# Optimization experiments

Measured on AMD Instinct MI355X. Metric: run time of the kernel, lower is better.

The kernel has to match this reference:

```python
import jax, jax.numpy as jnp
import numpy as np
import math

B, T, D = 2, 1024, 256
N, H = 1024, 8
HD = N // H
K = 32
STEPS = 2
VOCAB = 32000
TWO_PI = 2.0 * math.pi


def _ln(x, g, b):
    mu = x.mean(-1, keepdims=True)
    var = ((x - mu) ** 2).mean(-1, keepdims=True)
    return (x - mu) / jnp.sqrt(var + 1e-5) * g + b


def _gelu(x):
    # torch nn.GELU default = exact erf form
    return jax.nn.gelu(x, approximate=False)


def _forward(tokens, emb, field_init, Wq, Wv, mW1, mb1, mW2, mb2, base_metric,
             decoder, hebbian, fW1, fb1, fW2, fb2, g1, b1, g2, b2, gf, bf, Wl, bl):
    x = emb[tokens] + field_init  # [B,T,D]
    # quantized RoPE (BDH): freqs quantized in pairs, phases mod 1
    freqs = 1.0 / (2.0 ** 16) ** (jnp.floor(jnp.arange(D) / 2) * 2.0 / D) / TWO_PI  # [D]
    phases = (jnp.arange(T, dtype=jnp.float32)[:, None] * freqs[None, :]) % 1.0 * TWO_PI  # [T,D]
    cos, sin = jnp.cos(phases)[None], jnp.sin(phases)[None]
    x_rot = jnp.stack([-x[..., 1::2], x[..., ::2]], axis=-1).reshape(x.shape)
    x = x * cos + x_rot * sin

    # window j of token t covers padded positions t..t+K-1 == original t-(K-1)..t (causal)
    win_idx = jnp.arange(T)[:, None] + jnp.arange(K)[None, :]  # [T,K]

    def interaction(y):
        qs = jax.nn.relu(jnp.einsum('btd,hde->bthe', y, Wq))  # [B,T,H,HD] sparse query
        vs = jax.nn.relu(jnp.einsum('btd,hde->bthe', y, Wv))  # [B,T,H,HD] sparse value
        # dynamic diagonal metric from field signature
        qf = qs.reshape(B, T, N)
        sig = qf.mean(1) + qf[:, ::8].mean(1) * 0.5  # T >= 8 branch
        mod = _gelu(sig @ mW1 + mb1) @ mW2 + mb2  # [B,H*HD]
        metric = jax.nn.softplus(base_metric[None] + 0.1 * mod.reshape(B, H, HD)) + 1e-6
        # causal k-window extraction (unfold equivalent)
        qp = jnp.pad(qs, ((0, 0), (K - 1, 0), (0, 0), (0, 0)))
        vp = jnp.pad(vs, ((0, 0), (K - 1, 0), (0, 0), (0, 0)))
        qw = qp[:, win_idx].transpose(0, 1, 3, 2, 4)  # [B,T,H,K,HD]
        vw = vp[:, win_idx].transpose(0, 1, 3, 2, 4)
        diff = qs[:, :, :, None, :] - qw
        dist = jnp.sqrt(jnp.sum(metric[:, None, :, None, :] * diff ** 2, -1) + 1e-8)  # [B,T,H,K]
        infl = jnp.exp(-dist)
        infl = infl / (infl.sum(-1, keepdims=True) + 1e-8)
        ctx = jnp.einsum('bthk,bthkd->bthd', infl, vw)
        # Hebbian memory contraction (eval mode: state is fixed buffer)
        qn = qs / jnp.maximum(jnp.linalg.norm(qs, axis=-1, keepdims=True), 1e-12)
        ctx = ctx + jnp.einsum('bthd,hde->bthe', qn, hebbian)
        # multiplicative gating + decode
        return (qs * ctx).reshape(B, T, N) @ decoder

    for _ in range(STEPS):  # fixed evolution steps (eval, dropout off)
        dx = interaction(_ln(x, g1, b1)) + (_gelu(_ln(x, g2, b2) @ fW1 + fb1) @ fW2 + fb2)
        x = x + dx
    return _ln(x, gf, bf) @ Wl + bl  # [B,T,VOCAB]


def setup_inputs() -> dict:
    key = jax.random.key(0)
    ks = jax.random.split(key, 12)
    s = 0.02
    return {
        'tokens': jax.random.randint(ks[0], (B, T), 0, VOCAB),
        'emb': jax.random.normal(ks[1], (VOCAB, D)) * s,
        'field_init': jax.random.normal(ks[2], (1, 1, D)) * s,
        'Wq': jax.random.normal(ks[3], (H, D, HD)) * s,
        'Wv': jax.random.normal(ks[4], (H, D, HD)) * s,
        'mW1': jax.random.normal(ks[5], (N, N // 2)) * s,
        'mb1': jnp.zeros((N // 2,)),
        'mW2': jax.random.normal(ks[6], (N // 2, H * HD)) * s,
        'mb2': jnp.zeros((H * HD,)),
        'base_metric': jnp.ones((H, HD)) * 0.1,
        'decoder': jax.random.normal(ks[7], (N, D)) * s,
        'hebbian': jax.random.normal(ks[8], (H, HD, HD)) * 0.01,
        'fW1': jax.random.normal(ks[9], (D, 4 * D)) * s,
        'fb1': jnp.zeros((4 * D,)),
        'fW2': jax.random.normal(ks[10], (4 * D, D)) * s,
        'fb2': jnp.zeros((D,)),
        'g1': jnp.ones((D,)), 'b1': jnp.zeros((D,)),
        'g2': jnp.ones((D,)), 'b2': jnp.zeros((D,)),
        'gf': jnp.ones((D,)), 'bf': jnp.zeros((D,)),
        'Wl': jax.random.normal(ks[11], (D, VOCAB)) * s,
        'bl': jnp.zeros((VOCAB,)),
    }


def reference(tokens, emb, field_init, Wq, Wv, mW1, mb1, mW2, mb2, base_metric,
              decoder, hebbian, fW1, fb1, fW2, fb2, g1, b1, g2, b2, gf, bf, Wl, bl):
    return _forward(tokens, emb, field_init, Wq, Wv, mW1, mb1, mW2, mb2, base_metric,
                    decoder, hebbian, fW1, fb1, fW2, fb2, g1, b1, g2, b2, gf, bf, Wl, bl)
```

## Files before the change

### kernel.cpp

```cpp
#include <hip/hip_runtime.h>
#include <hip/hip_bf16.h>
#include <math.h>

#define B_ 2
#define T_ 1024
#define D_ 256
#define N_ 1024
#define H_ 8
#define HD_ 128
#define K_ 32
#define VOCAB_ 32000
#define TC_ 16

typedef __attribute__((ext_vector_type(8))) short short8v;
typedef __attribute__((ext_vector_type(4))) float f32x4;

static __device__ __forceinline__ float geluf(float x) {
    return 0.5f * x * (1.0f + erff(x * 0.70710678118654752f));
}

static __device__ __forceinline__ ushort f2bf(float f) {
    unsigned u = __builtin_bit_cast(unsigned, f);
    u += 0x7fff + ((u >> 16) & 1);
    return (ushort)(u >> 16);
}

static __device__ __forceinline__ float bf2f(ushort u) {
    unsigned v = ((unsigned)u) << 16;
    return __builtin_bit_cast(float, v);
}

__global__ void embed_rope_ln_kernel(const int* __restrict__ tokens,
                                     const float* __restrict__ emb,
                                     const float* __restrict__ field_init,
                                     const float* __restrict__ g1, const float* __restrict__ b1,
                                     const float* __restrict__ g2, const float* __restrict__ b2,
                                     float* __restrict__ x,
                                     ushort* __restrict__ y1, ushort* __restrict__ y2) {
    int bt = blockIdx.x;
    int d = threadIdx.x;
    int t = bt & (T_ - 1);
    int tok = tokens[bt];
    float v = emb[(long)tok * D_ + d] + field_init[d];
    float partner = __shfl_xor(v, 1);
    float rot = (d & 1) ? partner : -partner;
    float freq = exp2f(-0.0625f * (float)(d & ~1)) * (1.0f / 6.283185307179586f);
    float ph = fmodf((float)t * freq, 1.0f) * 6.283185307179586f;
    v = v * cosf(ph) + rot * sinf(ph);
    long i = (long)bt * D_ + d;
    x[i] = v;
    __shared__ float red[4];
    int lane = d & 63, wid = d >> 6;
    float s = v;
    #pragma unroll
    for (int off = 32; off; off >>= 1) s += __shfl_xor(s, off);
    if (lane == 0) red[wid] = s;
    __syncthreads();
    float mu = (red[0] + red[1] + red[2] + red[3]) * (1.0f / D_);
    float dv = v - mu;
    float s2 = dv * dv;
    #pragma unroll
    for (int off = 32; off; off >>= 1) s2 += __shfl_xor(s2, off);
    __syncthreads();
    if (lane == 0) red[wid] = s2;
    __syncthreads();
    float var = (red[0] + red[1] + red[2] + red[3]) * (1.0f / D_);
    float rstd = rsqrtf(var + 1e-5f);
    float nv = dv * rstd;
    y1[i] = f2bf(nv * g1[d] + b1[d]);
    y2[i] = f2bf(nv * g2[d] + b2[d]);
}

__global__ void ln_kernel(float* __restrict__ x,
                          const float* __restrict__ addA, const float* __restrict__ addB,
                          const float* __restrict__ g1, const float* __restrict__ b1,
                          const float* __restrict__ g2, const float* __restrict__ b2,
                          ushort* __restrict__ y1, ushort* __restrict__ y2) {
    int row = blockIdx.x;
    int d = threadIdx.x;
    long i = (long)row * D_ + d;
    float v = x[i] + addA[i] + addB[i];
    x[i] = v;
    __shared__ float red[4];
    int lane = d & 63, wid = d >> 6;
    float s = v;
    #pragma unroll
    for (int off = 32; off; off >>= 1) s += __shfl_xor(s, off);
    if (lane == 0) red[wid] = s;
    __syncthreads();
    float mu = (red[0] + red[1] + red[2] + red[3]) * (1.0f / D_);
    float dv = v - mu;
    float s2 = dv * dv;
    #pragma unroll
    for (int off = 32; off; off >>= 1) s2 += __shfl_xor(s2, off);
    __syncthreads();
    if (lane == 0) red[wid] = s2;
    __syncthreads();
    float var = (red[0] + red[1] + red[2] + red[3]) * (1.0f / D_);
    float rstd = rsqrtf(var + 1e-5f);
    float nv = dv * rstd;
    y1[i] = f2bf(nv * g1[d] + b1[d]);
    if (y2) y2[i] = f2bf(nv * g2[d] + b2[d]);
}

static __device__ __forceinline__ void tcast_tile(
    const float* __restrict__ in, ushort* __restrict__ out,
    int R, int C, int ry, int cx) {
    __shared__ float sm[64][65];
    int r0 = ry * 64, c0 = cx * 64;
    int tx = threadIdx.x & 63, ty = threadIdx.x >> 6;
    #pragma unroll
    for (int i = 0; i < 16; ++i) {
        int r = i * 4 + ty;
        sm[r][tx] = in[(long)(r0 + r) * C + c0 + tx];
    }
    __syncthreads();
    #pragma unroll
    for (int i = 0; i < 16; ++i) {
        int c = i * 4 + ty;
        out[(long)(c0 + c) * R + r0 + tx] = f2bf(sm[tx][c]);
    }
}

__global__ __launch_bounds__(256) void tcast_kernel(
    const float* __restrict__ in, ushort* __restrict__ out, int R, int C) {
    tcast_tile(in, out, R, C, blockIdx.y, blockIdx.x);
}

struct TcastBatch {
    const float* in[8];
    ushort* out[8];
    long inS[8], outS[8];
    int cb[8], rb[8], R[8], C[8];
    int cum[9];
};

__global__ __launch_bounds__(256) void tcast_all_kernel(TcastBatch tb) {
    int bid = blockIdx.x;
    int d = 0;
    #pragma unroll
    for (int i = 0; i < 8; ++i) if (bid >= tb.cum[i + 1]) d = i + 1;
    int local = bid - tb.cum[d];
    int bpz = tb.cb[d] * tb.rb[d];
    int z = local / bpz;
    int rem = local - z * bpz;
    int cx = rem % tb.cb[d], ry = rem / tb.cb[d];
    tcast_tile(tb.in[d] + z * tb.inS[d], tb.out[d] + z * tb.outS[d],
               tb.R[d], tb.C[d], ry, cx);
}

#define LDK 72
#define CSTR 132

__device__ __forceinline__ void gemm128_core(
    const ushort* __restrict__ A, int lda,
    const ushort* __restrict__ Bt, int ldb,
    const float* __restrict__ bias, void* __restrict__ Cout, int ldc,
    int Kd, int bx, int by, int act, int outbf) {
    __shared__ __align__(16) ushort As[128 * LDK];
    __shared__ __align__(16) ushort Bs[128 * LDK];
    int tid = threadIdx.x;
    int wid = tid >> 6, lane = tid & 63;
    int brow = by * 128, bcol = bx * 128;
    int wr = wid >> 1, wc = wid & 1;
    f32x4 acc[4][4] = {};
    for (int k0 = 0; k0 < Kd; k0 += 64) {
        __syncthreads();
        #pragma unroll
        for (int j = 0; j < 4; ++j) {
            int idx = tid + j * 256;
            int r = idx >> 3, sgm = idx & 7;
            *(short8v*)&As[r * LDK + sgm * 8] =
                *(const short8v*)&A[(long)(brow + r) * lda + k0 + sgm * 8];
            *(short8v*)&Bs[r * LDK + sgm * 8] =
                *(const short8v*)&Bt[(long)(bcol + r) * ldb + k0 + sgm * 8];
        }
        __syncthreads();
        #pragma unroll
        for (int kk = 0; kk < 2; ++kk) {
            short8v af[4], bfv[4];
            #pragma unroll
            for (int m = 0; m < 4; ++m)
                af[m] = *(const short8v*)&As[(wr * 64 + m * 16 + (lane & 15)) * LDK + kk * 32 + (lane >> 4) * 8];
            #pragma unroll
            for (int n = 0; n < 4; ++n)
                bfv[n] = *(const short8v*)&Bs[(wc * 64 + n * 16 + (lane & 15)) * LDK + kk * 32 + (lane >> 4) * 8];
            #pragma unroll
            for (int m = 0; m < 4; ++m)
                #pragma unroll
                for (int n = 0; n < 4; ++n)
                    acc[m][n] = __builtin_amdgcn_mfma_f32_16x16x32_bf16(af[m], bfv[n], acc[m][n], 0, 0, 0);
        }
    }
    float* Cs = (float*)As;
    #pragma unroll
    for (int chunk = 0; chunk < 4; ++chunk) {
        __syncthreads();
        if (wr == (chunk >> 1)) {
            #pragma unroll
            for (int mm = 0; mm < 2; ++mm) {
                int m = (chunk & 1) * 2 + mm;
                int lr0 = mm * 16 + ((lane >> 4) << 2);
                #pragma unroll
                for (int n = 0; n < 4; ++n) {
                    int lcol = wc * 64 + n * 16 + (lane & 15);
                    #pragma unroll
                    for (int j = 0; j < 4; ++j)
                        Cs[(lr0 + j) * CSTR + lcol] = acc[m][n][j];
                }
            }
        }
        __syncthreads();
        int lrow = tid >> 3, f4 = tid & 7;
        long grow = brow + chunk * 32 + lrow;
        if (outbf) {
            #pragma unroll
            for (int u = 0; u < 2; ++u) {
                int c0i = (f4 + u * 8) * 8;
                uint pk[4];
                #pragma unroll
                for (int q = 0; q < 4; ++q) {
                    int cc = c0i + 2 * q;
                    float v0 = Cs[lrow * CSTR + cc]     + (bias ? bias[bcol + cc] : 0.0f);
                    float v1 = Cs[lrow * CSTR + cc + 1] + (bias ? bias[bcol + cc + 1] : 0.0f);
                    if (act == 1) { v0 = fmaxf(v0, 0.0f); v1 = fmaxf(v1, 0.0f); }
                    else if (act == 2) { v0 = geluf(v0); v1 = geluf(v1); }
                    pk[q] = (uint)f2bf(v0) | ((uint)f2bf(v1) << 16);
                }
                *(uint4*)&((ushort*)Cout)[grow * ldc + bcol + c0i] = *(uint4*)pk;
            }
        } else {
            #pragma unroll
            for (int u = 0; u < 4; ++u) {
                int c0i = (f4 + u * 8) * 4;
                float vv[4];
                #pragma unroll
                for (int q = 0; q < 4; ++q) {
                    float v = Cs[lrow * CSTR + c0i + q] + (bias ? bias[bcol + c0i + q] : 0.0f);
                    if (act == 1) v = fmaxf(v, 0.0f);
                    else if (act == 2) v = geluf(v);
                    vv[q] = v;
                }
                *(float4*)&((float*)Cout)[grow * ldc + bcol + c0i] = *(float4*)vv;
            }
        }
    }
}

__global__ __launch_bounds__(256) void gemm3_kernel(
    const ushort* __restrict__ y1, const ushort* __restrict__ y2,
    const ushort* __restrict__ WqT, const ushort* __restrict__ WvT, const ushort* __restrict__ fW1T,
    const float* __restrict__ fb1,
    ushort* __restrict__ qs, ushort* __restrict__ vs, ushort* __restrict__ ffnh) {
    int z = blockIdx.z;
    const ushort* A = (z == 2) ? y2 : y1;
    const ushort* Bt = (z == 0) ? WqT : (z == 1) ? WvT : fW1T;
    const float* bias = (z == 2) ? fb1 : nullptr;
    void* C = (z == 0) ? (void*)qs : (z == 1) ? (void*)vs : (void*)ffnh;
    gemm128_core(A, 256, Bt, 256, bias, C, 1024, 256, blockIdx.x, blockIdx.y, (z == 2) ? 2 : 1, 1);
}

__global__ __launch_bounds__(256) void heb_gemm_kernel(
    const ushort* __restrict__ qn, const ushort* __restrict__ hebT,
    float* __restrict__ hebout) {
    int h = blockIdx.z;
    gemm128_core(qn + h * HD_, 1024, hebT + (long)h * HD_ * HD_, HD_,
                 nullptr, hebout + h * HD_, 1024, HD_, 0, blockIdx.y, 0, 0);
}

__global__ __launch_bounds__(256) void vocab_kernel(
    const ushort* __restrict__ yf, const ushort* __restrict__ WlT,
    const float* __restrict__ bl, float* __restrict__ out) {
    int g = blockIdx.x;
    int nid = (g & 7) * 500 + (g >> 3);
    gemm128_core(yf, 256, WlT, 256, bl, out, VOCAB_, 256, nid >> 4, nid & 15, 0, 0);
}

__global__ __launch_bounds__(256) void gemm2_kernel(
    const ushort* __restrict__ gated, const ushort* __restrict__ ffnh,
    const ushort* __restrict__ decT, const ushort* __restrict__ fW2T,
    const float* __restrict__ fb2,
    float* __restrict__ dec_out, float* __restrict__ ffn_out) {
    int z = blockIdx.z;
    const ushort* A = z ? ffnh : gated;
    const ushort* Bt = z ? fW2T : decT;
    const float* bias = z ? fb2 : nullptr;
    float* C = z ? ffn_out : dec_out;
    const int Kd = 1024, N = 256;
    __shared__ __align__(16) ushort As[64 * LDK];
    __shared__ __align__(16) ushort Bs[64 * LDK];
    int tid = threadIdx.x;
    int wid = tid >> 6, lane = tid & 63;
    int brow = blockIdx.y * 64, bcol = blockIdx.x * 64;
    int wr = wid >> 1, wc = wid & 1;
    f32x4 acc[2][2] = {};
    for (int k0 = 0; k0 < Kd; k0 += 64) {
        __syncthreads();
        #pragma unroll
        for (int j = 0; j < 2; ++j) {
            int idx = tid + j * 256;
            int r = idx >> 3, sgm = idx & 7;
            *(short8v*)&As[r * LDK + sgm * 8] =
                *(const short8v*)&A[(long)(brow + r) * Kd + k0 + sgm * 8];
            *(short8v*)&Bs[r * LDK + sgm * 8] =
                *(const short8v*)&Bt[(long)(bcol + r) * Kd + k0 + sgm * 8];
        }
        __syncthreads();
        #pragma unroll
        for (int kk = 0; kk < 2; ++kk) {
            short8v af[2], bfv[2];
            #pragma unroll
            for (int m = 0; m < 2; ++m)
                af[m] = *(const short8v*)&As[(wr * 32 + m * 16 + (lane & 15)) * LDK + kk * 32 + (lane >> 4) * 8];
            #pragma unroll
            for (int n = 0; n < 2; ++n)
                bfv[n] = *(const short8v*)&Bs[(wc * 32 + n * 16 + (lane & 15)) * LDK + kk * 32 + (lane >> 4) * 8];
            #pragma unroll
            for (int m = 0; m < 2; ++m)
                #pragma unroll
                for (int n = 0; n < 2; ++n)
                    acc[m][n] = __builtin_amdgcn_mfma_f32_16x16x32_bf16(af[m], bfv[n], acc[m][n], 0, 0, 0);
        }
    }
    int r0 = brow + wr * 32 + ((lane >> 4) << 2);
    int c0 = bcol + wc * 32 + (lane & 15);
    #pragma unroll
    for (int n = 0; n < 2; ++n) {
        int col = c0 + n * 16;
        float bv = bias ? bias[col] : 0.0f;
        #pragma unroll
        for (int m = 0; m < 2; ++m)
            #pragma unroll
            for (int j = 0; j < 4; ++j)
                C[(long)(r0 + m * 16 + j) * N + col] = acc[m][n][j] + bv;
    }
}

__global__ void sig_stage1(const ushort* __restrict__ qs,
                           float* __restrict__ ps, float* __restrict__ ps8) {
    int bn = blockIdx.x * 256 + threadIdx.x;
    int tc = blockIdx.y;
    int b = bn >> 10, n = bn & 1023;
    float s = 0.f, s8 = 0.f;
    int t0 = tc * (T_ / TC_);
    for (int t = t0; t < t0 + T_ / TC_; ++t) {
        float v = bf2f(qs[((long)(b * T_ + t) << 10) + n]);
        s += v;
        if ((t & 7) == 0) s8 += v;
    }
    ps[tc * 2048 + bn] = s;
    ps8[tc * 2048 + bn] = s8;
}

__global__ void sig_stage2(const float* __restrict__ ps, const float* __restrict__ ps8,
                           float* __restrict__ sig) {
    int bn = blockIdx.x * 256 + threadIdx.x;
    float s = 0.f, s8 = 0.f;
    for (int tc = 0; tc < TC_; ++tc) { s += ps[tc * 2048 + bn]; s8 += ps8[tc * 2048 + bn]; }
    sig[bn] = s * (1.0f / T_) + 0.5f * s8 * (1.0f / (T_ / 8));
}

__global__ __launch_bounds__(256) void mlp1_kernel(
    const float* __restrict__ sig, const ushort* __restrict__ mW1T,
    const float* __restrict__ mb1, float* __restrict__ hid) {
    int widx = blockIdx.x * 4 + (threadIdx.x >> 6);
    int b = widx >> 9, j = widx & 511;
    int lane = threadIdx.x & 63;
    const float* sg = sig + b * 1024;
    const ushort* w = mW1T + (long)j * 1024;
    float acc = 0.f;
    #pragma unroll
    for (int c = 0; c < 2; ++c) {
        int n0 = c * 512 + lane * 8;
        short8v wv = *(const short8v*)&w[n0];
        float4 s0 = *(const float4*)&sg[n0];
        float4 s1 = *(const float4*)&sg[n0 + 4];
        acc += bf2f((ushort)wv[0]) * s0.x + bf2f((ushort)wv[1]) * s0.y
             + bf2f((ushort)wv[2]) * s0.z + bf2f((ushort)wv[3]) * s0.w
             + bf2f((ushort)wv[4]) * s1.x + bf2f((ushort)wv[5]) * s1.y
             + bf2f((ushort)wv[6]) * s1.z + bf2f((ushort)wv[7]) * s1.w;
    }
    #pragma unroll
    for (int off = 32; off; off >>= 1) acc += __shfl_xor(acc, off);
    if (lane == 0) hid[b * 512 + j] = geluf(acc + mb1[j]);
}

__global__ __launch_bounds__(256) void mlp2_kernel(
    const float* __restrict__ hid, const ushort* __restrict__ mW2T,
    const float* __restrict__ mb2, const float* __restrict__ base_metric,
    float* __restrict__ metric) {
    int widx = blockIdx.x * 4 + (threadIdx.x >> 6);
    int b = widx >> 10, i = widx & 1023;
    int lane = threadIdx.x & 63;
    const float* hd = hid + b * 512;
    const ushort* w = mW2T + (long)i * 512;
    int j0 = lane * 8;
    short8v wv = *(const short8v*)&w[j0];
    float4 h0 = *(const float4*)&hd[j0];
    float4 h1 = *(const float4*)&hd[j0 + 4];
    float acc = bf2f((ushort)wv[0]) * h0.x + bf2f((ushort)wv[1]) * h0.y
              + bf2f((ushort)wv[2]) * h0.z + bf2f((ushort)wv[3]) * h0.w
              + bf2f((ushort)wv[4]) * h1.x + bf2f((ushort)wv[5]) * h1.y
              + bf2f((ushort)wv[6]) * h1.z + bf2f((ushort)wv[7]) * h1.w;
    #pragma unroll
    for (int off = 32; off; off >>= 1) acc += __shfl_xor(acc, off);
    if (lane == 0) {
        float v = base_metric[i] + 0.1f * (acc + mb2[i]);
        float sp = fmaxf(v, 0.f) + log1pf(expf(-fabsf(v)));
        metric[b * 1024 + i] = sp + 1e-6f;
    }
}

__global__ __launch_bounds__(256) void qn_kernel(
    const ushort* __restrict__ qs, ushort* __restrict__ qn) {
    int bt = blockIdx.x >> 1;
    int h = (blockIdx.x & 1) * 4 + (threadIdx.x >> 6);
    int lane = threadIdx.x & 63;
    long rowbase = (long)bt * N_ + h * HD_;
    uint qp = *(const uint*)&qs[rowbase + 2 * lane];
    float q0 = bf2f((ushort)(qp & 0xffff)), q1 = bf2f((ushort)(qp >> 16));
    float nv = q0 * q0 + q1 * q1;
    #pragma unroll
    for (int off = 32; off; off >>= 1) nv += __shfl_xor(nv, off);
    float invn = 1.0f / fmaxf(sqrtf(nv), 1e-12f);
    uint outp = (uint)f2bf(q0 * invn) | ((uint)f2bf(q1 * invn) << 16);
    *(uint*)&qn[rowbase + 2 * lane] = outp;
}

#define WLDR 67

__global__ __launch_bounds__(256) void window_kernel(
    const ushort* __restrict__ qs, const ushort* __restrict__ vs,
    const float* __restrict__ metric, const float* __restrict__ hebout,
    ushort* __restrict__ gated) {
    int tile = blockIdx.x, h = blockIdx.y, b = blockIdx.z;
    int t0 = tile * 32;
    int tid = threadIdx.x;
    __shared__ uint Qw[63 * WLDR];
    __shared__ uint Vw[63 * WLDR];
    __shared__ float smf[HD_];
    if (tid < HD_) smf[tid] = sqrtf(metric[(b * H_ + h) * HD_ + tid]);
    __syncthreads();
    for (int i = tid; i < 63 * 64; i += 256) {
        int r = i >> 6, c = i & 63;
        int grow = t0 - 31 + r;
        uint qv = 0, vv = 0;
        if (grow >= 0) {
            long base = ((long)(b * T_ + grow) * N_ + h * HD_) >> 1;
            qv = ((const uint*)qs)[base + c];
            vv = ((const uint*)vs)[base + c];
        }
        float q0 = bf2f((ushort)(qv & 0xffff)) * smf[2 * c];
        float q1 = bf2f((ushort)(qv >> 16)) * smf[2 * c + 1];
        Qw[r * WLDR + c] = (uint)f2bf(q0) | ((uint)f2bf(q1) << 16);
        Vw[r * WLDR + c] = vv;
    }
    __syncthreads();
    int w = tid >> 6, lane = tid & 63;
    int k = lane & 31, half = lane >> 5;
    #pragma unroll 2
    for (int i = 0; i < 8; ++i) {
        int lt = w * 8 + i;
        int t = t0 + lt;
        const uint* qtrow = &Qw[(lt + 31) * WLDR + half * 32];
        const uint* qsrow = &Qw[(lt + k) * WLDR + half * 32];
        float val = 0.f;
        #pragma unroll
        for (int j = 0; j < 32; ++j) {
            uint a = qtrow[j], s = qsrow[j];
            float d0 = bf2f((ushort)(a & 0xffff)) - bf2f((ushort)(s & 0xffff));
            float d1 = bf2f((ushort)(a >> 16)) - bf2f((ushort)(s >> 16));
            val = fmaf(d0, d0, val);
            val = fmaf(d1, d1, val);
        }
        val += __shfl_xor(val, 32);
        float infl = __expf(-sqrtf(val + 1e-8f));
        float ws = infl;
        #pragma unroll
        for (int off = 16; off; off >>= 1) ws += __shfl_xor(ws, off);
        float wk = infl / (ws + 1e-8f);
        float c0 = 0.f, c1 = 0.f;
        #pragma unroll
        for (int kk = 0; kk < 32; ++kk) {
            float wkk = __shfl(wk, kk);
            uint vu = Vw[(lt + kk) * WLDR + lane];
            c0 = fmaf(wkk, bf2f((ushort)(vu & 0xffff)), c0);
            c1 = fmaf(wkk, bf2f((ushort)(vu >> 16)), c1);
        }
        long rowb = (long)(b * T_ + t) * N_ + h * HD_;
        float2 hb = *(const float2*)&hebout[rowb + 2 * lane];
        uint qo = *(const uint*)&qs[rowb + 2 * lane];
        c0 += hb.x; c1 += hb.y;
        float g0 = bf2f((ushort)(qo & 0xffff)) * c0;
        float g1 = bf2f((ushort)(qo >> 16)) * c1;
        *(uint*)&gated[rowb + 2 * lane] = (uint)f2bf(g0) | ((uint)f2bf(g1) << 16);
    }
}

extern "C" void kernel_launch(void* const* d_in, const int* in_sizes, int n_in,
                              void* d_out, int out_size, void* d_ws, size_t ws_size,
                              hipStream_t stream) {
    const int*   tokens      = (const int*)  d_in[0];
    const float* emb         = (const float*)d_in[1];
    const float* field_init  = (const float*)d_in[2];
    const float* Wq          = (const float*)d_in[3];
    const float* Wv          = (const float*)d_in[4];
    const float* mW1         = (const float*)d_in[5];
    const float* mb1         = (const float*)d_in[6];
    const float* mW2         = (const float*)d_in[7];
    const float* mb2         = (const float*)d_in[8];
    const float* base_metric = (const float*)d_in[9];
    const float* decoder     = (const float*)d_in[10];
    const float* hebbian     = (const float*)d_in[11];
    const float* fW1         = (const float*)d_in[12];
    const float* fb1         = (const float*)d_in[13];
    const float* fW2         = (const float*)d_in[14];
    const float* fb2         = (const float*)d_in[15];
    const float* g1          = (const float*)d_in[16];
    const float* b1          = (const float*)d_in[17];
    const float* g2          = (const float*)d_in[18];
    const float* b2          = (const float*)d_in[19];
    const float* gf          = (const float*)d_in[20];
    const float* bf          = (const float*)d_in[21];
    const float* Wl          = (const float*)d_in[22];
    const float* bl          = (const float*)d_in[23];
    float* out = (float*)d_out;

    char* wp = (char*)d_ws;
    auto alloc = [&](size_t bytes) { char* p = wp; wp += (bytes + 255) & ~255UL; return p; };
    float*  x        = (float*) alloc(524288 * 4);
    ushort* y1_bf    = (ushort*)alloc(524288 * 2);
    ushort* y2_bf    = (ushort*)alloc(524288 * 2);
    ushort* yf_bf    = (ushort*)alloc(524288 * 2);
    ushort* qs_bf    = (ushort*)alloc(2097152 * 2);
    ushort* vs_bf    = (ushort*)alloc(2097152 * 2);
    ushort* gated_bf = (ushort*)alloc(2097152 * 2);
    ushort* ffnh_bf  = (ushort*)alloc(2097152 * 2);
    float*  dec_out  = (float*) alloc(524288 * 4);
    float*  ffn_out  = (float*) alloc(524288 * 4);
    ushort* qn_bf    = (ushort*)alloc(2097152 * 2);
    float*  hebout   = (float*) alloc(2097152 * 4);
    ushort* WqT      = (ushort*)alloc(262144 * 2);
    ushort* WvT      = (ushort*)alloc(262144 * 2);
    ushort* decT     = (ushort*)alloc(262144 * 2);
    ushort* fW1T     = (ushort*)alloc(262144 * 2);
    ushort* fW2T     = (ushort*)alloc(262144 * 2);
    ushort* mW1T     = (ushort*)alloc(524288 * 2);
    ushort* mW2T     = (ushort*)alloc(524288 * 2);
    ushort* hebT     = (ushort*)alloc(131072 * 2);
    float*  ps       = (float*) alloc(TC_ * 2048 * 4);
    float*  ps8      = (float*) alloc(TC_ * 2048 * 4);
    float*  sigb     = (float*) alloc(2048 * 4);
    float*  hid      = (float*) alloc(1024 * 4);
    float*  metricb  = (float*) alloc(2048 * 4);
    ushort* WlT      = (ushort*)qs_bf;

    TcastBatch tb;
    const float* tin[8]  = {Wq, Wv, decoder, fW1, fW2, mW1, mW2, hebbian};
    ushort*      tout[8] = {WqT, WvT, decT, fW1T, fW2T, mW1T, mW2T, hebT};
    long tinS[8]  = {256 * 128, 256 * 128, 0, 0, 0, 0, 0, 128 * 128};
    long toutS[8] = {128 * 256, 128 * 256, 0, 0, 0, 0, 0, 128 * 128};
    int tR[8] = {256, 256, 1024, 256, 1024, 1024, 512, 128};
    int tC[8] = {128, 128, 256, 1024, 256, 512, 1024, 128};
    int cum = 0;
    tb.cum[0] = 0;
    for (int i = 0; i < 8; ++i) {
        tb.in[i] = tin[i]; tb.out[i] = tout[i];
        tb.inS[i] = tinS[i]; tb.outS[i] = toutS[i];
        tb.R[i] = tR[i]; tb.C[i] = tC[i];
        tb.cb[i] = tC[i] / 64; tb.rb[i] = tR[i] / 64;
        int zc = (i == 0 || i == 1 || i == 7) ? 8 : 1;
        cum += tb.cb[i] * tb.rb[i] * zc;
        tb.cum[i + 1] = cum;
    }
    tcast_all_kernel<<<cum, 256, 0, stream>>>(tb);

    embed_rope_ln_kernel<<<B_ * T_, 256, 0, stream>>>(
        tokens, emb, field_init, g1, b1, g2, b2, x, y1_bf, y2_bf);

    for (int step = 0; step < 2; ++step) {
        if (step == 1)
            ln_kernel<<<B_ * T_, 256, 0, stream>>>(
                x, dec_out, ffn_out, g1, b1, g2, b2, y1_bf, y2_bf);
        gemm3_kernel<<<dim3(8, 16, 3), 256, 0, stream>>>(
            y1_bf, y2_bf, WqT, WvT, fW1T, fb1, qs_bf, vs_bf, ffnh_bf);
        qn_kernel<<<B_ * T_ * 2, 256, 0, stream>>>(qs_bf, qn_bf);
        heb_gemm_kernel<<<dim3(1, 16, 8), 256, 0, stream>>>(qn_bf, hebT, hebout);
        sig_stage1<<<dim3(8, TC_), 256, 0, stream>>>(qs_bf, ps, ps8);
        sig_stage2<<<8, 256, 0, stream>>>(ps, ps8, sigb);
        mlp1_kernel<<<256, 256, 0, stream>>>(sigb, mW1T, mb1, hid);
        mlp2_kernel<<<512, 256, 0, stream>>>(hid, mW2T, mb2, base_metric, metricb);
        window_kernel<<<dim3(T_ / 32, H_, B_), 256, 0, stream>>>(
            qs_bf, vs_bf, metricb, hebout, gated_bf);
        gemm2_kernel<<<dim3(4, 32, 2), 256, 0, stream>>>(
            gated_bf, ffnh_bf, decT, fW2T, fb2, dec_out, ffn_out);
    }
    ln_kernel<<<B_ * T_, 256, 0, stream>>>(
        x, dec_out, ffn_out, gf, bf, nullptr, nullptr, yf_bf, nullptr);
    tcast_kernel<<<dim3(500, 4), 256, 0, stream>>>(Wl, WlT, 256, VOCAB_);
    vocab_kernel<<<4000, 256, 0, stream>>>(yf_bf, WlT, bl, out);
}
```

Before: 317.8 us.

## Fuse signature reduction into Q GEMM and Hebbian matmul into window kernel

Per-column signature partial sums are now computed in the Q-projection GEMM epilogue, and the final reduction is done inside mlp1. This removes the sig_stage1/sig_stage2 kernels and a re-read of qs. The q-normalization and Hebbian matmul are folded into window_kernel as scalar FMAs from shared memory, which drops the qn and heb_gemm kernels and the fp32 hebout round trip. The cost is that the Hebbian product now runs on scalar ALUs instead of MFMA, and window_kernel gains register and LDS pressure. The GEMM core is also templated on activation, output type and signature flags.

After: 312.9 us. Within noise of the previous version (-1.6%).

```diff
diff --git a/kernel.cpp b/kernel.cpp
--- a/kernel.cpp
+++ b/kernel.cpp
@@ -10,7 +10,6 @@
 #define HD_ 128
 #define K_ 32
 #define VOCAB_ 32000
-#define TC_ 16
 
 typedef __attribute__((ext_vector_type(8))) short short8v;
 typedef __attribute__((ext_vector_type(4))) float f32x4;
@@ -152,11 +151,13 @@
 #define LDK 72
 #define CSTR 132
 
+template<int ACT, int OUTBF, int SIG>
 __device__ __forceinline__ void gemm128_core(
     const ushort* __restrict__ A, int lda,
     const ushort* __restrict__ Bt, int ldb,
     const float* __restrict__ bias, void* __restrict__ Cout, int ldc,
-    int Kd, int bx, int by, int act, int outbf) {
+    int Kd, int bx, int by,
+    float* __restrict__ psOut, float* __restrict__ ps8Out) {
     __shared__ __align__(16) ushort As[128 * LDK];
     __shared__ __align__(16) ushort Bs[128 * LDK];
     int tid = threadIdx.x;
@@ -193,6 +194,7 @@
         }
     }
     float* Cs = (float*)As;
+    float cs = 0.f, cs8 = 0.f;
     #pragma unroll
     for (int chunk = 0; chunk < 4; ++chunk) {
         __syncthreads();
@@ -213,7 +215,7 @@
         __syncthreads();
         int lrow = tid >> 3, f4 = tid & 7;
         long grow = brow + chunk * 32 + lrow;
-        if (outbf) {
+        if (OUTBF) {
             #pragma unroll
             for (int u = 0; u < 2; ++u) {
                 int c0i = (f4 + u * 8) * 8;
@@ -223,8 +225,8 @@
                     int cc = c0i + 2 * q;
                     float v0 = Cs[lrow * CSTR + cc]     + (bias ? bias[bcol + cc] : 0.0f);
                     float v1 = Cs[lrow * CSTR + cc + 1] + (bias ? bias[bcol + cc + 1] : 0.0f);
-                    if (act == 1) { v0 = fmaxf(v0, 0.0f); v1 = fmaxf(v1, 0.0f); }
-                    else if (act == 2) { v0 = geluf(v0); v1 = geluf(v1); }
+                    if (ACT == 1) { v0 = fmaxf(v0, 0.0f); v1 = fmaxf(v1, 0.0f); }
+                    else if (ACT == 2) { v0 = geluf(v0); v1 = geluf(v1); }
                     pk[q] = (uint)f2bf(v0) | ((uint)f2bf(v1) << 16);
                 }
                 *(uint4*)&((ushort*)Cout)[grow * ldc + bcol + c0i] = *(uint4*)pk;
@@ -237,13 +239,25 @@
                 #pragma unroll
                 for (int q = 0; q < 4; ++q) {
                     float v = Cs[lrow * CSTR + c0i + q] + (bias ? bias[bcol + c0i + q] : 0.0f);
-                    if (act == 1) v = fmaxf(v, 0.0f);
-                    else if (act == 2) v = geluf(v);
+                    if (ACT == 1) v = fmaxf(v, 0.0f);
+                    else if (ACT == 2) v = geluf(v);
                     vv[q] = v;
                 }
                 *(float4*)&((float*)Cout)[grow * ldc + bcol + c0i] = *(float4*)vv;
             }
         }
+        if (SIG && tid < 128) {
+            #pragma unroll
+            for (int r = 0; r < 32; ++r) {
+                float vr = fmaxf(Cs[r * CSTR + tid], 0.0f);
+                cs += vr;
+                if ((r & 7) == 0) cs8 += vr;
+            }
+        }
+    }
+    if (SIG && tid < 128) {
+        psOut[by * 1024 + bcol + tid] = cs;
+        ps8Out[by * 1024 + bcol + tid] = cs8;
     }
 }
 
@@ -251,21 +265,18 @@
     const ushort* __restrict__ y1, const ushort* __restrict__ y2,
     const ushort* __restrict__ WqT, const ushort* __restrict__ WvT, const ushort* __restrict__ fW1T,
     const float* __restrict__ fb1,
-    ushort* __restrict__ qs, ushort* __restrict__ vs, ushort* __restrict__ ffnh) {
+    ushort* __restrict__ qs, ushort* __restrict__ vs, ushort* __restrict__ ffnh,
+    float* __restrict__ ps, float* __restrict__ ps8) {
     int z = blockIdx.z;
-    const ushort* A = (z == 2) ? y2 : y1;
-    const ushort* Bt = (z == 0) ? WqT : (z == 1) ? WvT : fW1T;
-    const float* bias = (z == 2) ? fb1 : nullptr;
-    void* C = (z == 0) ? (void*)qs : (z == 1) ? (void*)vs : (void*)ffnh;
-    gemm128_core(A, 256, Bt, 256, bias, C, 1024, 256, blockIdx.x, blockIdx.y, (z == 2) ? 2 : 1, 1);
-}
-
-__global__ __launch_bounds__(256) void heb_gemm_kernel(
-    const ushort* __restrict__ qn, const ushort* __restrict__ hebT,
-    float* __restrict__ hebout) {
-    int h = blockIdx.z;
-    gemm128_core(qn + h * HD_, 1024, hebT + (long)h * HD_ * HD_, HD_,
-                 nullptr, hebout + h * HD_, 1024, HD_, 0, blockIdx.y, 0, 0);
+    if (z == 0)
+        gemm128_core<1, 1, 1>(y1, 256, WqT, 256, nullptr, qs, 1024, 256,
+                              blockIdx.x, blockIdx.y, ps, ps8);
+    else if (z == 1)
+        gemm128_core<1, 1, 0>(y1, 256, WvT, 256, nullptr, vs, 1024, 256,
+                              blockIdx.x, blockIdx.y, nullptr, nullptr);
+    else
+        gemm128_core<2, 1, 0>(y2, 256, fW1T, 256, fb1, ffnh, 1024, 256,
+                              blockIdx.x, blockIdx.y, nullptr, nullptr);
 }
 
 __global__ __launch_bounds__(256) void vocab_kernel(
@@ -273,7 +284,8 @@
     const float* __restrict__ bl, float* __restrict__ out) {
     int g = blockIdx.x;
     int nid = (g & 7) * 500 + (g >> 3);
-    gemm128_core(yf, 256, WlT, 256, bl, out, VOCAB_, 256, nid >> 4, nid & 15, 0, 0);
+    gemm128_core<0, 0, 0>(yf, 256, WlT, 256, bl, out, VOCAB_, 256,
+                          nid >> 4, nid & 15, nullptr, nullptr);
 }
 
 __global__ __launch_bounds__(256) void gemm2_kernel(
@@ -336,49 +348,35 @@
     }
 }
 
-__global__ void sig_stage1(const ushort* __restrict__ qs,
-                           float* __restrict__ ps, float* __restrict__ ps8) {
-    int bn = blockIdx.x * 256 + threadIdx.x;
-    int tc = blockIdx.y;
-    int b = bn >> 10, n = bn & 1023;
-    float s = 0.f, s8 = 0.f;
-    int t0 = tc * (T_ / TC_);
-    for (int t = t0; t < t0 + T_ / TC_; ++t) {
-        float v = bf2f(qs[((long)(b * T_ + t) << 10) + n]);
-        s += v;
-        if ((t & 7) == 0) s8 += v;
-    }
-    ps[tc * 2048 + bn] = s;
-    ps8[tc * 2048 + bn] = s8;
-}
-
-__global__ void sig_stage2(const float* __restrict__ ps, const float* __restrict__ ps8,
-                           float* __restrict__ sig) {
-    int bn = blockIdx.x * 256 + threadIdx.x;
-    float s = 0.f, s8 = 0.f;
-    for (int tc = 0; tc < TC_; ++tc) { s += ps[tc * 2048 + bn]; s8 += ps8[tc * 2048 + bn]; }
-    sig[bn] = s * (1.0f / T_) + 0.5f * s8 * (1.0f / (T_ / 8));
-}
-
 __global__ __launch_bounds__(256) void mlp1_kernel(
-    const float* __restrict__ sig, const ushort* __restrict__ mW1T,
-    const float* __restrict__ mb1, float* __restrict__ hid) {
-    int widx = blockIdx.x * 4 + (threadIdx.x >> 6);
-    int b = widx >> 9, j = widx & 511;
-    int lane = threadIdx.x & 63;
-    const float* sg = sig + b * 1024;
-    const ushort* w = mW1T + (long)j * 1024;
+    const float* __restrict__ ps, const float* __restrict__ ps8,
+    const ushort* __restrict__ mW1T, const float* __restrict__ mb1,
+    float* __restrict__ hid) {
+    int blk = blockIdx.x;
+    int b = blk >> 7;
+    __shared__ float sig_l[1024];
+    int tid = threadIdx.x;
+    for (int c = tid; c < 1024; c += 256) {
+        float s = 0.f, s8 = 0.f;
+        #pragma unroll
+        for (int by8 = 0; by8 < 8; ++by8) {
+            s += ps[(b * 8 + by8) * 1024 + c];
+            s8 += ps8[(b * 8 + by8) * 1024 + c];
+        }
+        sig_l[c] = s * (1.0f / 1024.0f) + 0.5f * s8 * (1.0f / 128.0f);
+    }
+    __syncthreads();
+    int wv = tid >> 6, lane = tid & 63;
+    int j = (blk & 127) * 4 + wv;
+    const ushort* wrow = mW1T + (long)j * 1024;
     float acc = 0.f;
     #pragma unroll
-    for (int c = 0; c < 2; ++c) {
-        int n0 = c * 512 + lane * 8;
-        short8v wv = *(const short8v*)&w[n0];
-        float4 s0 = *(const float4*)&sg[n0];
-        float4 s1 = *(const float4*)&sg[n0 + 4];
-        acc += bf2f((ushort)wv[0]) * s0.x + bf2f((ushort)wv[1]) * s0.y
-             + bf2f((ushort)wv[2]) * s0.z + bf2f((ushort)wv[3]) * s0.w
-             + bf2f((ushort)wv[4]) * s1.x + bf2f((ushort)wv[5]) * s1.y
-             + bf2f((ushort)wv[6]) * s1.z + bf2f((ushort)wv[7]) * s1.w;
+    for (int c2 = 0; c2 < 4; ++c2) {
+        int n0 = c2 * 256 + lane * 4;
+        float4 sv = *(const float4*)&sig_l[n0];
+        ushort4 w4 = *(const ushort4*)&wrow[n0];
+        acc += bf2f(w4.x) * sv.x + bf2f(w4.y) * sv.y
+             + bf2f(w4.z) * sv.z + bf2f(w4.w) * sv.w;
     }
     #pragma unroll
     for (int off = 32; off; off >>= 1) acc += __shfl_xor(acc, off);
@@ -411,33 +409,18 @@
     }
 }
 
-__global__ __launch_bounds__(256) void qn_kernel(
-    const ushort* __restrict__ qs, ushort* __restrict__ qn) {
-    int bt = blockIdx.x >> 1;
-    int h = (blockIdx.x & 1) * 4 + (threadIdx.x >> 6);
-    int lane = threadIdx.x & 63;
-    long rowbase = (long)bt * N_ + h * HD_;
-    uint qp = *(const uint*)&qs[rowbase + 2 * lane];
-    float q0 = bf2f((ushort)(qp & 0xffff)), q1 = bf2f((ushort)(qp >> 16));
-    float nv = q0 * q0 + q1 * q1;
-    #pragma unroll
-    for (int off = 32; off; off >>= 1) nv += __shfl_xor(nv, off);
-    float invn = 1.0f / fmaxf(sqrtf(nv), 1e-12f);
-    uint outp = (uint)f2bf(q0 * invn) | ((uint)f2bf(q1 * invn) << 16);
-    *(uint*)&qn[rowbase + 2 * lane] = outp;
-}
-
 #define WLDR 67
 
 __global__ __launch_bounds__(256) void window_kernel(
     const ushort* __restrict__ qs, const ushort* __restrict__ vs,
-    const float* __restrict__ metric, const float* __restrict__ hebout,
+    const float* __restrict__ metric, const ushort* __restrict__ hebT,
     ushort* __restrict__ gated) {
     int tile = blockIdx.x, h = blockIdx.y, b = blockIdx.z;
     int t0 = tile * 32;
     int tid = threadIdx.x;
     __shared__ uint Qw[63 * WLDR];
     __shared__ uint Vw[63 * WLDR];
+    __shared__ uint Qr[32 * 64];
     __shared__ float smf[HD_];
     if (tid < HD_) smf[tid] = sqrtf(metric[(b * H_ + h) * HD_ + tid]);
     __syncthreads();
@@ -454,10 +437,40 @@
         float q1 = bf2f((ushort)(qv >> 16)) * smf[2 * c + 1];
         Qw[r * WLDR + c] = (uint)f2bf(q0) | ((uint)f2bf(q1) << 16);
         Vw[r * WLDR + c] = vv;
+        if (r >= 31) Qr[(r - 31) * 64 + c] = qv;
     }
     __syncthreads();
     int w = tid >> 6, lane = tid & 63;
     int k = lane & 31, half = lane >> 5;
+    float invn[8];
+    #pragma unroll
+    for (int ri = 0; ri < 8; ++ri) {
+        uint u = Qr[(w * 8 + ri) * 64 + lane];
+        float a0 = bf2f((ushort)(u & 0xffff)), a1 = bf2f((ushort)(u >> 16));
+        float nv = a0 * a0 + a1 * a1;
+        #pragma unroll
+        for (int off = 32; off; off >>= 1) nv += __shfl_xor(nv, off);
+        invn[ri] = 1.0f / fmaxf(sqrtf(nv), 1e-12f);
+    }
+    const ushort* hb = hebT + (long)h * HD_ * HD_;
+    float hacc0[8] = {}, hacc1[8] = {};
+    for (int dv = 0; dv < 16; ++dv) {
+        short8v h0 = *(const short8v*)&hb[(2 * lane) * HD_ + dv * 8];
+        short8v h1 = *(const short8v*)&hb[(2 * lane + 1) * HD_ + dv * 8];
+        #pragma unroll
+        for (int ri = 0; ri < 8; ++ri) {
+            uint4 qu = *(const uint4*)&Qr[(w * 8 + ri) * 64 + dv * 4];
+            float qd[8] = {bf2f((ushort)(qu.x & 0xffff)), bf2f((ushort)(qu.x >> 16)),
+                           bf2f((ushort)(qu.y & 0xffff)), bf2f((ushort)(qu.y >> 16)),
+                           bf2f((ushort)(qu.z & 0xffff)), bf2f((ushort)(qu.z >> 16)),
+                           bf2f((ushort)(qu.w & 0xffff)), bf2f((ushort)(qu.w >> 16))};
+            #pragma unroll
+            for (int j = 0; j < 8; ++j) {
+                hacc0[ri] = fmaf(qd[j], bf2f((ushort)h0[j]), hacc0[ri]);
+                hacc1[ri] = fmaf(qd[j], bf2f((ushort)h1[j]), hacc1[ri]);
+            }
+        }
+    }
     #pragma unroll 2
     for (int i = 0; i < 8; ++i) {
         int lt = w * 8 + i;
@@ -479,7 +492,7 @@
         #pragma unroll
         for (int off = 16; off; off >>= 1) ws += __shfl_xor(ws, off);
         float wk = infl / (ws + 1e-8f);
-        float c0 = 0.f, c1 = 0.f;
+        float c0 = hacc0[i] * invn[i], c1 = hacc1[i] * invn[i];
         #pragma unroll
         for (int kk = 0; kk < 32; ++kk) {
             float wkk = __shfl(wk, kk);
@@ -487,12 +500,10 @@
             c0 = fmaf(wkk, bf2f((ushort)(vu & 0xffff)), c0);
             c1 = fmaf(wkk, bf2f((ushort)(vu >> 16)), c1);
         }
-        long rowb = (long)(b * T_ + t) * N_ + h * HD_;
-        float2 hb = *(const float2*)&hebout[rowb + 2 * lane];
-        uint qo = *(const uint*)&qs[rowb + 2 * lane];
-        c0 += hb.x; c1 += hb.y;
+        uint qo = Qr[lt * 64 + lane];
         float g0 = bf2f((ushort)(qo & 0xffff)) * c0;
         float g1 = bf2f((ushort)(qo >> 16)) * c1;
+        long rowb = (long)(b * T_ + t) * N_ + h * HD_;
         *(uint*)&gated[rowb + 2 * lane] = (uint)f2bf(g0) | ((uint)f2bf(g1) << 16);
     }
 }
@@ -538,8 +549,6 @@
     ushort* ffnh_bf  = (ushort*)alloc(2097152 * 2);
     float*  dec_out  = (float*) alloc(524288 * 4);
     float*  ffn_out  = (float*) alloc(524288 * 4);
-    ushort* qn_bf    = (ushort*)alloc(2097152 * 2);
-    float*  hebout   = (float*) alloc(2097152 * 4);
     ushort* WqT      = (ushort*)alloc(262144 * 2);
     ushort* WvT      = (ushort*)alloc(262144 * 2);
     ushort* decT     = (ushort*)alloc(262144 * 2);
@@ -548,9 +557,8 @@
     ushort* mW1T     = (ushort*)alloc(524288 * 2);
     ushort* mW2T     = (ushort*)alloc(524288 * 2);
     ushort* hebT     = (ushort*)alloc(131072 * 2);
-    float*  ps       = (float*) alloc(TC_ * 2048 * 4);
-    float*  ps8      = (float*) alloc(TC_ * 2048 * 4);
-    float*  sigb     = (float*) alloc(2048 * 4);
+    float*  ps       = (float*) alloc(16 * 1024 * 4);
+    float*  ps8      = (float*) alloc(16 * 1024 * 4);
     float*  hid      = (float*) alloc(1024 * 4);
     float*  metricb  = (float*) alloc(2048 * 4);
     ushort* WlT      = (ushort*)qs_bf;
@@ -583,15 +591,11 @@
             ln_kernel<<<B_ * T_, 256, 0, stream>>>(
                 x, dec_out, ffn_out, g1, b1, g2, b2, y1_bf, y2_bf);
         gemm3_kernel<<<dim3(8, 16, 3), 256, 0, stream>>>(
-            y1_bf, y2_bf, WqT, WvT, fW1T, fb1, qs_bf, vs_bf, ffnh_bf);
-        qn_kernel<<<B_ * T_ * 2, 256, 0, stream>>>(qs_bf, qn_bf);
-        heb_gemm_kernel<<<dim3(1, 16, 8), 256, 0, stream>>>(qn_bf, hebT, hebout);
-        sig_stage1<<<dim3(8, TC_), 256, 0, stream>>>(qs_bf, ps, ps8);
-        sig_stage2<<<8, 256, 0, stream>>>(ps, ps8, sigb);
-        mlp1_kernel<<<256, 256, 0, stream>>>(sigb, mW1T, mb1, hid);
+            y1_bf, y2_bf, WqT, WvT, fW1T, fb1, qs_bf, vs_bf, ffnh_bf, ps, ps8);
+        mlp1_kernel<<<256, 256, 0, stream>>>(ps, ps8, mW1T, mb1, hid);
         mlp2_kernel<<<512, 256, 0, stream>>>(hid, mW2T, mb2, base_metric, metricb);
         window_kernel<<<dim3(T_ / 32, H_, B_), 256, 0, stream>>>(
-            qs_bf, vs_bf, metricb, hebout, gated_bf);
+            qs_bf, vs_bf, metricb, hebT, gated_bf);
         gemm2_kernel<<<dim3(4, 32, 2), 256, 0, stream>>>(
             gated_bf, ffnh_bf, decT, fW2T, fb2, dec_out, ffn_out);
     }
```
